# Optimization experiments

Measured on AMD Instinct MI355X. Metric: run time of the kernel, lower is better.

The kernel has to match this reference:

```python
import jax, jax.numpy as jnp
import numpy as np

L, B, D, H = 2048, 2, 1024, 16
DK = D // H
SCALE = DK ** -0.5


def setup_inputs() -> dict:
    key = jax.random.key(0)
    ks = jax.random.split(key, 11)
    w_std = D ** -0.5
    return {
        "query": jax.random.normal(ks[0], (L, B, D), dtype=jnp.float32),
        "key": jax.random.normal(ks[1], (L, B, D), dtype=jnp.float32),
        "value": jax.random.normal(ks[2], (L, B, D), dtype=jnp.float32),
        "WQ_w": jax.random.normal(ks[3], (D, D), dtype=jnp.float32) * w_std,
        "WQ_b": jnp.zeros((D,), dtype=jnp.float32),
        "WK_w": jax.random.normal(ks[4], (D, D), dtype=jnp.float32) * w_std,
        "WK_b": jnp.zeros((D,), dtype=jnp.float32),
        "WV_w": jax.random.normal(ks[5], (D, D), dtype=jnp.float32) * w_std,
        "WV_b": jnp.zeros((D,), dtype=jnp.float32),
        "WO_w": jax.random.normal(ks[6], (D, D), dtype=jnp.float32) * w_std,
        "WO_b": jnp.zeros((D,), dtype=jnp.float32),
    }


def reference(query, key, value, WQ_w, WQ_b, WK_w, WK_b, WV_w, WV_b, WO_w, WO_b):
    tgt_len, batch, _ = query.shape
    src_len = key.shape[0]
    # linear projections (torch Linear: x @ W^T + b)
    q = (query @ WQ_w.T + WQ_b) * SCALE            # [L, B, D]
    k = key @ WK_w.T + WK_b                        # [S, B, D]
    v = value @ WV_w.T + WV_b                      # [S, B, D]
    # split heads: [len, B, D] -> [B*H, len, DK]
    q = q.reshape(tgt_len, batch * H, DK).transpose(1, 0, 2)
    k = k.reshape(src_len, batch * H, DK).transpose(1, 0, 2)
    v = v.reshape(src_len, batch * H, DK).transpose(1, 0, 2)
    # attention scores and softmax (full [B*H, L, S] matrix, as in the original)
    scores = jnp.einsum('nld,nsd->nls', q, k)      # [B*H, L, S]
    probs = jax.nn.softmax(scores, axis=-1)
    out = jnp.einsum('nls,nsd->nld', probs, v)     # [B*H, L, DK]
    # merge heads: [B*H, L, DK] -> [L, B, D]
    out = out.transpose(1, 0, 2).reshape(tgt_len, batch, D)
    return out @ WO_w.T + WO_b
```

## Files before the change

kernel.cpp:

```cpp
#include <hip/hip_runtime.h>
#include <hip/hip_fp16.h>

#define LL 2048
#define BB 2
#define DD 1024
#define HH 16
#define DKK 64

typedef _Float16 h8 __attribute__((ext_vector_type(8)));
typedef _Float16 h4 __attribute__((ext_vector_type(4)));
typedef float f4 __attribute__((ext_vector_type(4)));
typedef float f16v __attribute__((ext_vector_type(16)));

#define BAR() do {                                              \
    asm volatile("s_waitcnt lgkmcnt(0)" ::: "memory");          \
    __builtin_amdgcn_s_barrier();                               \
    asm volatile("" ::: "memory");                              \
} while (0)

__device__ __forceinline__ void gload_lds16(const void* g, void* l) {
    __builtin_amdgcn_global_load_lds(
        (const __attribute__((address_space(1))) void*)g,
        (__attribute__((address_space(3))) void*)l, 16, 0, 0);
}

__device__ __forceinline__ unsigned pack2h(float a, float b) {
    union { _Float16 h[2]; unsigned u; } x;
    x.h[0] = (_Float16)a; x.h[1] = (_Float16)b;
    return x.u;
}

__global__ __launch_bounds__(256) void cvt_all(
    const float* __restrict__ x0, const float* __restrict__ x1,
    const float* __restrict__ x2, const float* __restrict__ w0,
    const float* __restrict__ w1, const float* __restrict__ w2,
    const float* __restrict__ w3,
    _Float16* __restrict__ y0, _Float16* __restrict__ y1,
    _Float16* __restrict__ y2, _Float16* __restrict__ z0,
    _Float16* __restrict__ z1, _Float16* __restrict__ z2,
    _Float16* __restrict__ z3)
{
    const int sel = blockIdx.y;
    if (sel >= 3 && blockIdx.x >= 512) return;
    const float* src = (sel == 0) ? x0 : (sel == 1) ? x1 : (sel == 2) ? x2
                     : (sel == 3) ? w0 : (sel == 4) ? w1 : (sel == 5) ? w2 : w3;
    _Float16* dst = (sel == 0) ? y0 : (sel == 1) ? y1 : (sel == 2) ? y2
                  : (sel == 3) ? z0 : (sel == 4) ? z1 : (sel == 5) ? z2 : z3;
    const int i = (blockIdx.x * 256 + threadIdx.x) * 8;
    f4 a = *(const f4*)(src + i);
    f4 b = *(const f4*)(src + i + 4);
    h8 o = {(_Float16)a.x, (_Float16)a.y, (_Float16)a.z, (_Float16)a.w,
            (_Float16)b.x, (_Float16)b.y, (_Float16)b.z, (_Float16)b.w};
    *(h8*)(dst + i) = o;
}

__global__ __launch_bounds__(256) void qkv_proj(
    const _Float16* __restrict__ xq, const _Float16* __restrict__ xk,
    const _Float16* __restrict__ xv,
    const _Float16* __restrict__ wq, const float* __restrict__ bq,
    const _Float16* __restrict__ wk, const float* __restrict__ bk,
    const _Float16* __restrict__ wv, const float* __restrict__ bv,
    _Float16* __restrict__ qh, _Float16* __restrict__ kh,
    _Float16* __restrict__ vth)
{
    const int mode = blockIdx.z;
    const _Float16* X    = (mode == 0) ? xq : (mode == 1) ? xk : xv;
    const _Float16* W    = (mode == 0) ? wq : (mode == 1) ? wk : wv;
    const float*    bias = (mode == 0) ? bq : (mode == 1) ? bk : bv;

    __shared__ alignas(16) _Float16 a_sm[128 * 32];
    __shared__ alignas(16) _Float16 b_sm[128 * 32];

    const int tid  = threadIdx.x;
    const int lane = tid & 63;
    const int wave = tid >> 6;
    const int wm = (wave & 1) * 64;
    const int wn = (wave >> 1) * 64;
    const int m0 = blockIdx.x * 128;
    const int n0 = blockIdx.y * 128;

    const int srow = tid >> 2;
    const int scol = (tid & 3) * 8;
    const int lds_base = wave * 512;

    f4 acc[4][4];
    #pragma unroll
    for (int i = 0; i < 4; i++)
        #pragma unroll
        for (int j = 0; j < 4; j++)
            #pragma unroll
            for (int r = 0; r < 4; r++) acc[i][j][r] = 0.f;

    const int fr = lane & 15;
    const int fk = (lane >> 4) * 8;

    for (int k0 = 0; k0 < DD; k0 += 32) {
        gload_lds16(X + (size_t)(m0 + srow) * DD + k0 + scol,       &a_sm[lds_base]);
        gload_lds16(X + (size_t)(m0 + 64 + srow) * DD + k0 + scol,  &a_sm[2048 + lds_base]);
        gload_lds16(W + (size_t)(n0 + srow) * DD + k0 + scol,       &b_sm[lds_base]);
        gload_lds16(W + (size_t)(n0 + 64 + srow) * DD + k0 + scol,  &b_sm[2048 + lds_base]);
        __syncthreads();
        h8 af[4], bfr[4];
        #pragma unroll
        for (int i = 0; i < 4; i++) af[i]  = *(const h8*)&a_sm[(wm + i * 16 + fr) * 32 + fk];
        #pragma unroll
        for (int j = 0; j < 4; j++) bfr[j] = *(const h8*)&b_sm[(wn + j * 16 + fr) * 32 + fk];
        #pragma unroll
        for (int i = 0; i < 4; i++)
            #pragma unroll
            for (int j = 0; j < 4; j++)
                acc[i][j] = __builtin_amdgcn_mfma_f32_16x16x32_f16(af[i], bfr[j], acc[i][j], 0, 0, 0);
        __syncthreads();
    }

    const int colc = lane & 15;
    const int rowb = (lane >> 4) * 4;
    #pragma unroll
    for (int i = 0; i < 4; i++) {
        #pragma unroll
        for (int j = 0; j < 4; j++) {
            const int nn = n0 + wn + j * 16 + colc;
            const float bval = bias[nn];
            #pragma unroll
            for (int reg = 0; reg < 4; reg++) {
                const int mm = m0 + wm + i * 16 + rowb + reg;
                float v = acc[i][j][reg] + bval;
                const int b = mm & 1, l = mm >> 1;
                const int h = nn >> 6, dk = nn & 63;
                const int head = b * HH + h;
                if (mode == 0) {
                    v *= 0.1803368801111243f;
                    qh[((size_t)head * LL + l) * DKK + dk] = (_Float16)v;
                } else if (mode == 1) {
                    kh[((size_t)head * LL + l) * DKK + dk] = (_Float16)v;
                } else {
                    vth[((size_t)head * DKK + dk) * LL + l] = (_Float16)v;
                }
            }
        }
    }
}

__global__ __launch_bounds__(512, 4) void attn(
    const _Float16* __restrict__ qh, const _Float16* __restrict__ kh,
    const _Float16* __restrict__ vth, _Float16* __restrict__ oh)
{
    const int rb = blockIdx.y * 16 + blockIdx.x;
    const int lb = (rb & 7) * 64 + (rb >> 3);
    const int head = lb >> 4;
    const int q0   = (lb & 15) * 128;

    const int tid = threadIdx.x, lane = tid & 63, wave = tid >> 6;
    const int qstrip = wave & 3;
    const int sh     = wave >> 2;
    const int qw = q0 + qstrip * 32;

    __shared__ alignas(16) char smem[65536];

    const int rq = lane & 31;
    const int hi = lane >> 5;
    const int kb = hi * 8;
    const unsigned key = (unsigned)(rq & 7);

    const _Float16* khead  = kh  + (size_t)head * LL * DKK;
    const _Float16* vthead = vth + (size_t)head * DKK * LL;

    const int seg0 = wave * 2;
    auto stage = [&](int s0, unsigned koff, unsigned voff) {
        #pragma unroll
        for (int t = 0; t < 2; t++) {
            const int i = (seg0 + t) * 64 + lane;
            const int r = i >> 3, p = i & 7;
            gload_lds16(khead + (size_t)(s0 + r) * DKK + ((p ^ (r & 7)) << 3),
                        smem + koff + (unsigned)(seg0 + t) * 1024u);
        }
        #pragma unroll
        for (int t = 0; t < 2; t++) {
            const int i = (seg0 + t) * 64 + lane;
            const int r = i >> 4, p = i & 15;
            gload_lds16(vthead + (size_t)r * LL + s0 + ((p ^ (r & 7)) << 3),
                        smem + voff + (unsigned)(seg0 + t) * 1024u);
        }
    };

    stage(0, 0u, 16384u);

    const _Float16* qbase = qh + ((size_t)head * LL + qw + rq) * DKK;
    h8 qa[4];
    #pragma unroll
    for (int kf = 0; kf < 4; kf++) qa[kf] = *(const h8*)(qbase + kf * 16 + kb);

    f16v o0, o1;
    #pragma unroll
    for (int r = 0; r < 16; r++) { o0[r] = 0.f; o1[r] = 0.f; }
    float lsum = 0.f;

    asm volatile("s_waitcnt vmcnt(0)" ::: "memory");
    BAR();

    for (int it = 0; it < 16; ++it) {
        const unsigned cb = (unsigned)(it & 1) * 32768u;
        const unsigned nb = (unsigned)((it + 1) & 1) * 32768u;
        if (it < 15) stage((it + 1) * 128, nb, nb + 16384u);

        const char* kc = smem + cb;
        const char* vc = smem + cb + 16384u;

        f16v sc[2];
        #pragma unroll
        for (int st2 = 0; st2 < 2; st2++) {
            const int st = sh * 2 + st2;
            #pragma unroll
            for (int r = 0; r < 16; r++) sc[st2][r] = 0.f;
            #pragma unroll
            for (int kf = 0; kf < 4; kf++) {
                h8 kf8 = *(const h8*)(kc +
                    ((((unsigned)(st * 32 + rq) << 3) +
                      (((unsigned)(kf * 2 + hi)) ^ key)) << 4));
                sc[st2] = __builtin_amdgcn_mfma_f32_32x32x16_f16(kf8, qa[kf], sc[st2], 0, 0, 0);
            }
        }

        #pragma unroll
        for (int st2 = 0; st2 < 2; st2++) {
            const int st = sh * 2 + st2;
            float p[16];
            #pragma unroll
            for (int r = 0; r < 16; r++) {
                p[r] = __builtin_amdgcn_exp2f(sc[st2][r]);
                lsum += p[r];
            }
            unsigned w0[4], w1[4];
            #pragma unroll
            for (int g = 0; g < 4; g++) {
                w0[g] = pack2h(p[4 * g],     p[4 * g + 1]);
                w1[g] = pack2h(p[4 * g + 2], p[4 * g + 3]);
            }
            #pragma unroll
            for (int j = 0; j < 2; j++) {
                unsigned x0 = w0[2 * j], y0 = w0[2 * j + 1];
                unsigned x1 = w1[2 * j], y1 = w1[2 * j + 1];
                asm("v_permlane32_swap_b32 %0, %1" : "+v"(x0), "+v"(y0));
                asm("v_permlane32_swap_b32 %0, %1" : "+v"(x1), "+v"(y1));
                union { unsigned u[4]; h8 h; } pa;
                pa.u[0] = x0; pa.u[1] = x1; pa.u[2] = y0; pa.u[3] = y1;
                h8 b0 = *(const h8*)(vc +
                    ((((unsigned)rq << 4) +
                      (((unsigned)(st * 4 + j * 2 + hi)) ^ key)) << 4));
                h8 b1 = *(const h8*)(vc +
                    ((((unsigned)(32 + rq) << 4) +
                      (((unsigned)(st * 4 + j * 2 + hi)) ^ key)) << 4));
                o0 = __builtin_amdgcn_mfma_f32_32x32x16_f16(pa.h, b0, o0, 0, 0, 0);
                o1 = __builtin_amdgcn_mfma_f32_32x32x16_f16(pa.h, b1, o1, 0, 0, 0);
            }
        }

        asm volatile("s_waitcnt vmcnt(0)" ::: "memory");
        BAR();
    }

    lsum += __shfl_xor(lsum, 32, 64);

    float* xch = (float*)smem;
    float* lsp = (float*)(smem + 40960);
    float* myx = xch + ((qstrip * 64 + lane) * 33);
    if (sh) {
        #pragma unroll
        for (int r = 0; r < 16; r++) { myx[r] = o0[r]; myx[16 + r] = o1[r]; }
        myx[32] = lsum;
    }
    BAR();
    if (!sh) {
        #pragma unroll
        for (int r = 0; r < 16; r++) { o0[r] += myx[r]; o1[r] += myx[16 + r]; }
        lsum += myx[32];
        lsp[qstrip * 32 + rq] = 1.0f / lsum;
        asm volatile("s_waitcnt lgkmcnt(0)" ::: "memory");

        const int b = head >> 4, h = head & 15;
        #pragma unroll
        for (int r = 0; r < 16; r++) {
            const int qrow = (r & 3) + 8 * (r >> 2) + 4 * hi;
            const float inv = lsp[qstrip * 32 + qrow];
            const int ql = qw + qrow;
            const size_t base = (size_t)(ql * BB + b) * DD + h * DKK;
            oh[base + rq]      = (_Float16)(o0[r] * inv);
            oh[base + 32 + rq] = (_Float16)(o1[r] * inv);
        }
    }
}

__global__ __launch_bounds__(256) void out_proj(
    const _Float16* __restrict__ oh, const _Float16* __restrict__ wo,
    const float* __restrict__ bo, float* __restrict__ out)
{
    __shared__ alignas(16) _Float16 a_sm[64 * 32];
    __shared__ alignas(16) _Float16 b_sm[128 * 32];
    const int tid = threadIdx.x, lane = tid & 63, wave = tid >> 6;
    const int wm = (wave & 1) * 32, wn = (wave >> 1) * 64;
    const int m0 = blockIdx.x * 64, n0 = blockIdx.y * 128;

    const int srow = tid >> 2;
    const int scol = (tid & 3) * 8;
    const int lds_base = wave * 512;

    f4 acc[2][4];
    #pragma unroll
    for (int i = 0; i < 2; i++)
        #pragma unroll
        for (int j = 0; j < 4; j++)
            #pragma unroll
            for (int r = 0; r < 4; r++) acc[i][j][r] = 0.f;

    const int fr = lane & 15;
    const int fk = (lane >> 4) * 8;

    for (int k0 = 0; k0 < DD; k0 += 32) {
        gload_lds16(oh + (size_t)(m0 + srow) * DD + k0 + scol,      &a_sm[lds_base]);
        gload_lds16(wo + (size_t)(n0 + srow) * DD + k0 + scol,      &b_sm[lds_base]);
        gload_lds16(wo + (size_t)(n0 + 64 + srow) * DD + k0 + scol, &b_sm[2048 + lds_base]);
        __syncthreads();
        h8 af[2], bfr[4];
        #pragma unroll
        for (int i = 0; i < 2; i++) af[i]  = *(const h8*)&a_sm[(wm + i * 16 + fr) * 32 + fk];
        #pragma unroll
        for (int j = 0; j < 4; j++) bfr[j] = *(const h8*)&b_sm[(wn + j * 16 + fr) * 32 + fk];
        #pragma unroll
        for (int i = 0; i < 2; i++)
            #pragma unroll
            for (int j = 0; j < 4; j++)
                acc[i][j] = __builtin_amdgcn_mfma_f32_16x16x32_f16(af[i], bfr[j], acc[i][j], 0, 0, 0);
        __syncthreads();
    }

    const int colc = lane & 15;
    const int rowb = (lane >> 4) * 4;
    #pragma unroll
    for (int i = 0; i < 2; i++) {
        #pragma unroll
        for (int j = 0; j < 4; j++) {
            const int nn = n0 + wn + j * 16 + colc;
            const float bval = bo[nn];
            #pragma unroll
            for (int reg = 0; reg < 4; reg++) {
                const int mm = m0 + wm + i * 16 + rowb + reg;
                out[(size_t)mm * DD + nn] = acc[i][j][reg] + bval;
            }
        }
    }
}

extern "C" void kernel_launch(void* const* d_in, const int* in_sizes, int n_in,
                              void* d_out, int out_size, void* d_ws, size_t ws_size,
                              hipStream_t stream) {
    const float* qin = (const float*)d_in[0];
    const float* kin = (const float*)d_in[1];
    const float* vin = (const float*)d_in[2];
    const float* wq  = (const float*)d_in[3];
    const float* bq  = (const float*)d_in[4];
    const float* wk  = (const float*)d_in[5];
    const float* bk  = (const float*)d_in[6];
    const float* wv  = (const float*)d_in[7];
    const float* bv  = (const float*)d_in[8];
    const float* wo  = (const float*)d_in[9];
    const float* bo  = (const float*)d_in[10];

    const size_t seg = (size_t)32 * LL * DKK;
    _Float16* qh  = (_Float16*)d_ws;
    _Float16* kh  = qh + seg;
    _Float16* vth = kh + seg;
    _Float16* oh  = vth + seg;
    _Float16* wqh = oh + seg;
    _Float16* wkh = wqh + (size_t)DD * DD;
    _Float16* wvh = wkh + (size_t)DD * DD;
    _Float16* woh = wvh + (size_t)DD * DD;
    _Float16* xqh = woh + (size_t)DD * DD;
    _Float16* xkh = xqh + seg;
    _Float16* xvh = xkh + seg;

    hipLaunchKernelGGL(cvt_all, dim3(2048, 7), dim3(256), 0, stream,
                       qin, kin, vin, wq, wk, wv, wo,
                       xqh, xkh, xvh, wqh, wkh, wvh, woh);
    hipLaunchKernelGGL(qkv_proj, dim3(32, 8, 3), dim3(256), 0, stream,
                       xqh, xkh, xvh, wqh, bq, wkh, bk, wvh, bv, qh, kh, vth);
    hipLaunchKernelGGL(attn, dim3(16, 32), dim3(512), 0, stream, qh, kh, vth, oh);
    hipLaunchKernelGGL(out_proj, dim3(64, 8), dim3(256), 0, stream, oh, woh,
                       bo, (float*)d_out);
}
```

Baseline: 219.0 us.

## Deepen GEMM K-tiles to 64 with XOR-swizzled LDS, add setprio in attention

The QKV and output projection GEMMs now stage 64-wide K slices per barrier pair instead of 32. This halves the number of synchronisations, and an XOR swizzle on the global-to-LDS column placement avoids bank conflicts on the fragment reads. The attention kernel wraps its MFMA blocks in s_setprio raises and splits the softmax row-sum into two accumulators to shorten the dependency chain. LDS use per GEMM block doubles, which may reduce occupancy.

```diff
diff --git a/kernel.cpp b/kernel.cpp
--- a/kernel.cpp
+++ b/kernel.cpp
@@ -17,6 +17,8 @@
     __builtin_amdgcn_s_barrier();                               \
     asm volatile("" ::: "memory");                              \
 } while (0)
+
+#define VMCNT0() asm volatile("s_waitcnt vmcnt(0)" ::: "memory")
 
 __device__ __forceinline__ void gload_lds16(const void* g, void* l) {
     __builtin_amdgcn_global_load_lds(
@@ -68,8 +70,8 @@
     const _Float16* W    = (mode == 0) ? wq : (mode == 1) ? wk : wv;
     const float*    bias = (mode == 0) ? bq : (mode == 1) ? bk : bv;
 
-    __shared__ alignas(16) _Float16 a_sm[128 * 32];
-    __shared__ alignas(16) _Float16 b_sm[128 * 32];
+    __shared__ alignas(16) _Float16 a_sm[128 * 64];
+    __shared__ alignas(16) _Float16 b_sm[128 * 64];
 
     const int tid  = threadIdx.x;
     const int lane = tid & 63;
@@ -79,10 +81,6 @@
     const int m0 = blockIdx.x * 128;
     const int n0 = blockIdx.y * 128;
 
-    const int srow = tid >> 2;
-    const int scol = (tid & 3) * 8;
-    const int lds_base = wave * 512;
-
     f4 acc[4][4];
     #pragma unroll
     for (int i = 0; i < 4; i++)
@@ -92,24 +90,41 @@
             for (int r = 0; r < 4; r++) acc[i][j][r] = 0.f;
 
     const int fr = lane & 15;
-    const int fk = (lane >> 4) * 8;
-
-    for (int k0 = 0; k0 < DD; k0 += 32) {
-        gload_lds16(X + (size_t)(m0 + srow) * DD + k0 + scol,       &a_sm[lds_base]);
-        gload_lds16(X + (size_t)(m0 + 64 + srow) * DD + k0 + scol,  &a_sm[2048 + lds_base]);
-        gload_lds16(W + (size_t)(n0 + srow) * DD + k0 + scol,       &b_sm[lds_base]);
-        gload_lds16(W + (size_t)(n0 + 64 + srow) * DD + k0 + scol,  &b_sm[2048 + lds_base]);
+    const int l4 = lane >> 4;
+    const int key = fr & 7;
+
+    for (int k0 = 0; k0 < DD; k0 += 64) {
+        #pragma unroll
+        for (int rd = 0; rd < 4; rd++) {
+            const int id  = rd * 256 + tid;
+            const int row = id >> 3, p = id & 7;
+            const int gcol = k0 + ((p ^ (row & 7)) << 3);
+            gload_lds16(X + (size_t)(m0 + row) * DD + gcol,
+                        (char*)a_sm + rd * 4096 + wave * 1024);
+            gload_lds16(W + (size_t)(n0 + row) * DD + gcol,
+                        (char*)b_sm + rd * 4096 + wave * 1024);
+        }
         __syncthreads();
-        h8 af[4], bfr[4];
-        #pragma unroll
-        for (int i = 0; i < 4; i++) af[i]  = *(const h8*)&a_sm[(wm + i * 16 + fr) * 32 + fk];
-        #pragma unroll
-        for (int j = 0; j < 4; j++) bfr[j] = *(const h8*)&b_sm[(wn + j * 16 + fr) * 32 + fk];
-        #pragma unroll
-        for (int i = 0; i < 4; i++)
-            #pragma unroll
-            for (int j = 0; j < 4; j++)
-                acc[i][j] = __builtin_amdgcn_mfma_f32_16x16x32_f16(af[i], bfr[j], acc[i][j], 0, 0, 0);
+
+        #pragma unroll
+        for (int kk = 0; kk < 2; kk++) {
+            h8 af[4], bfr[4];
+            #pragma unroll
+            for (int i = 0; i < 4; i++) {
+                const int ra = wm + i * 16 + fr;
+                af[i] = *(const h8*)&a_sm[ra * 64 + (((kk * 4 + l4) ^ key) << 3)];
+            }
+            #pragma unroll
+            for (int j = 0; j < 4; j++) {
+                const int rb = wn + j * 16 + fr;
+                bfr[j] = *(const h8*)&b_sm[rb * 64 + (((kk * 4 + l4) ^ key) << 3)];
+            }
+            #pragma unroll
+            for (int i = 0; i < 4; i++)
+                #pragma unroll
+                for (int j = 0; j < 4; j++)
+                    acc[i][j] = __builtin_amdgcn_mfma_f32_16x16x32_f16(af[i], bfr[j], acc[i][j], 0, 0, 0);
+        }
         __syncthreads();
     }
 
@@ -193,9 +208,9 @@
     f16v o0, o1;
     #pragma unroll
     for (int r = 0; r < 16; r++) { o0[r] = 0.f; o1[r] = 0.f; }
-    float lsum = 0.f;
-
-    asm volatile("s_waitcnt vmcnt(0)" ::: "memory");
+    float lsum0 = 0.f, lsum1 = 0.f;
+
+    VMCNT0();
     BAR();
 
     for (int it = 0; it < 16; ++it) {
@@ -207,6 +222,7 @@
         const char* vc = smem + cb + 16384u;
 
         f16v sc[2];
+        __builtin_amdgcn_s_setprio(1);
         #pragma unroll
         for (int st2 = 0; st2 < 2; st2++) {
             const int st = sh * 2 + st2;
@@ -220,6 +236,7 @@
                 sc[st2] = __builtin_amdgcn_mfma_f32_32x32x16_f16(kf8, qa[kf], sc[st2], 0, 0, 0);
             }
         }
+        __builtin_amdgcn_s_setprio(0);
 
         #pragma unroll
         for (int st2 = 0; st2 < 2; st2++) {
@@ -228,7 +245,7 @@
             #pragma unroll
             for (int r = 0; r < 16; r++) {
                 p[r] = __builtin_amdgcn_exp2f(sc[st2][r]);
-                lsum += p[r];
+                if (r & 1) lsum1 += p[r]; else lsum0 += p[r];
             }
             unsigned w0[4], w1[4];
             #pragma unroll
@@ -236,6 +253,7 @@
                 w0[g] = pack2h(p[4 * g],     p[4 * g + 1]);
                 w1[g] = pack2h(p[4 * g + 2], p[4 * g + 3]);
             }
+            __builtin_amdgcn_s_setprio(1);
             #pragma unroll
             for (int j = 0; j < 2; j++) {
                 unsigned x0 = w0[2 * j], y0 = w0[2 * j + 1];
@@ -253,12 +271,14 @@
                 o0 = __builtin_amdgcn_mfma_f32_32x32x16_f16(pa.h, b0, o0, 0, 0, 0);
                 o1 = __builtin_amdgcn_mfma_f32_32x32x16_f16(pa.h, b1, o1, 0, 0, 0);
             }
-        }
-
-        asm volatile("s_waitcnt vmcnt(0)" ::: "memory");
+            __builtin_amdgcn_s_setprio(0);
+        }
+
+        VMCNT0();
         BAR();
     }
 
+    float lsum = lsum0 + lsum1;
     lsum += __shfl_xor(lsum, 32, 64);
 
     float* xch = (float*)smem;
@@ -294,16 +314,12 @@
     const _Float16* __restrict__ oh, const _Float16* __restrict__ wo,
     const float* __restrict__ bo, float* __restrict__ out)
 {
-    __shared__ alignas(16) _Float16 a_sm[64 * 32];
-    __shared__ alignas(16) _Float16 b_sm[128 * 32];
+    __shared__ alignas(16) _Float16 a_sm[64 * 64];
+    __shared__ alignas(16) _Float16 b_sm[128 * 64];
     const int tid = threadIdx.x, lane = tid & 63, wave = tid >> 6;
     const int wm = (wave & 1) * 32, wn = (wave >> 1) * 64;
     const int m0 = blockIdx.x * 64, n0 = blockIdx.y * 128;
 
-    const int srow = tid >> 2;
-    const int scol = (tid & 3) * 8;
-    const int lds_base = wave * 512;
-
     f4 acc[2][4];
     #pragma unroll
     for (int i = 0; i < 2; i++)
@@ -313,23 +329,45 @@
             for (int r = 0; r < 4; r++) acc[i][j][r] = 0.f;
 
     const int fr = lane & 15;
-    const int fk = (lane >> 4) * 8;
-
-    for (int k0 = 0; k0 < DD; k0 += 32) {
-        gload_lds16(oh + (size_t)(m0 + srow) * DD + k0 + scol,      &a_sm[lds_base]);
-        gload_lds16(wo + (size_t)(n0 + srow) * DD + k0 + scol,      &b_sm[lds_base]);
-        gload_lds16(wo + (size_t)(n0 + 64 + srow) * DD + k0 + scol, &b_sm[2048 + lds_base]);
+    const int l4 = lane >> 4;
+    const int key = fr & 7;
+
+    for (int k0 = 0; k0 < DD; k0 += 64) {
+        #pragma unroll
+        for (int rd = 0; rd < 2; rd++) {
+            const int id  = rd * 256 + tid;
+            const int row = id >> 3, p = id & 7;
+            gload_lds16(oh + (size_t)(m0 + row) * DD + k0 + ((p ^ (row & 7)) << 3),
+                        (char*)a_sm + rd * 4096 + wave * 1024);
+        }
+        #pragma unroll
+        for (int rd = 0; rd < 4; rd++) {
+            const int id  = rd * 256 + tid;
+            const int row = id >> 3, p = id & 7;
+            gload_lds16(wo + (size_t)(n0 + row) * DD + k0 + ((p ^ (row & 7)) << 3),
+                        (char*)b_sm + rd * 4096 + wave * 1024);
+        }
         __syncthreads();
-        h8 af[2], bfr[4];
-        #pragma unroll
-        for (int i = 0; i < 2; i++) af[i]  = *(const h8*)&a_sm[(wm + i * 16 + fr) * 32 + fk];
-        #pragma unroll
-        for (int j = 0; j < 4; j++) bfr[j] = *(const h8*)&b_sm[(wn + j * 16 + fr) * 32 + fk];
-        #pragma unroll
-        for (int i = 0; i < 2; i++)
-            #pragma unroll
-            for (int j = 0; j < 4; j++)
-                acc[i][j] = __builtin_amdgcn_mfma_f32_16x16x32_f16(af[i], bfr[j], acc[i][j], 0, 0, 0);
+
+        #pragma unroll
+        for (int kk = 0; kk < 2; kk++) {
+            h8 af[2], bfr[4];
+            #pragma unroll
+            for (int i = 0; i < 2; i++) {
+                const int ra = wm + i * 16 + fr;
+                af[i] = *(const h8*)&a_sm[ra * 64 + (((kk * 4 + l4) ^ key) << 3)];
+            }
+            #pragma unroll
+            for (int j = 0; j < 4; j++) {
+                const int rb = wn + j * 16 + fr;
+                bfr[j] = *(const h8*)&b_sm[rb * 64 + (((kk * 4 + l4) ^ key) << 3)];
+            }
+            #pragma unroll
+            for (int i = 0; i < 2; i++)
+                #pragma unroll
+                for (int j = 0; j < 4; j++)
+                    acc[i][j] = __builtin_amdgcn_mfma_f32_16x16x32_f16(af[i], bfr[j], acc[i][j], 0, 0, 0);
+        }
         __syncthreads();
     }
 
```

Result: no change. 223.3 us (+2.0%).
